# Optimization experiments

Measured on AMD Instinct MI355X. Metric: run time of the kernel, lower is better.

## Reference

```python
import jax, jax.numpy as jnp
import numpy as np

# ---- dims (match init_kwargs) ----
IMG = 128; PATCH = 16; GRID = IMG // PATCH; L = GRID * GRID  # 64 patches
D = 256            # embed_dim
EXP = 2; DIN = D * EXP          # d_inner = 512
DH = 64; H = DIN // DH          # 8 heads
G = 1; N = 64                   # n_groups, d_state
DCONV = 4
DEPTH = 2
NCLS = 1000
BATCH = 16
DINPROJ = 2 * DIN + 2 * G * N + H   # z | xBC | dt
CDIM = DIN + 2 * G * N              # conv channels
EPS = 1e-6

def _snake_indices():
    g = np.arange(L).reshape(GRID, GRID)
    g[1::2] = g[1::2, ::-1]
    return jnp.asarray(g.reshape(-1))

SNAKE = _snake_indices()

def rmsnorm(x, w):
    return x * jax.lax.rsqrt(jnp.mean(x * x, axis=-1, keepdims=True) + EPS) * w

def causal_depthwise_conv(x, w, b):
    # x: (B,L,C), w: (C,K) depthwise causal conv, then SiLU
    xp = jnp.pad(x, ((0, 0), (DCONV - 1, 0), (0, 0)))
    y = sum(xp[:, k:k + x.shape[1], :] * w[:, k] for k in range(DCONV))
    return jax.nn.silu(y + b)

def mamba_block(x, Win, cw, cb, dtb, Alog, Dp, gn, Wout):
    # Mamba-2/3 style selective scan block. x: (B,L,D)
    Bsz, Lx, _ = x.shape
    zxbcdt = x @ Win                                   # (B,L,DINPROJ)
    z   = zxbcdt[..., :DIN]
    xBC = zxbcdt[..., DIN:DIN + CDIM]
    dt  = jax.nn.softplus(zxbcdt[..., DIN + CDIM:] + dtb)   # (B,L,H)
    xBC = causal_depthwise_conv(xBC, cw, cb)
    xs = xBC[..., :DIN].reshape(Bsz, Lx, H, DH)
    Bm = xBC[..., DIN:DIN + G * N].reshape(Bsz, Lx, G, N)
    Cm = xBC[..., DIN + G * N:].reshape(Bsz, Lx, G, N)
    Bh = jnp.repeat(Bm, H // G, axis=2)                # (B,L,H,N)
    Ch = jnp.repeat(Cm, H // G, axis=2)
    decay = jnp.exp(dt * (-jnp.exp(Alog)))             # (B,L,H) in (0,1)
    dBx = jnp.einsum('blh,blhp,blhn->blhpn', dt, xs, Bh)
    def step(h, inp):
        d, u = inp
        h = d[..., None, None] * h + u
        return h, h
    _, hs = jax.lax.scan(step, jnp.zeros((Bsz, H, DH, N), x.dtype),
                         (jnp.moveaxis(decay, 1, 0), jnp.moveaxis(dBx, 1, 0)))
    hs = jnp.moveaxis(hs, 0, 1)                        # (B,L,H,DH,N)
    y = jnp.einsum('blhpn,blhn->blhp', hs, Ch) + Dp[None, None, :, None] * xs
    y = y.reshape(Bsz, Lx, DIN)
    y = rmsnorm(y * jax.nn.silu(z), gn)                # gated RMSNorm
    return y @ Wout                                    # (B,L,D)

def setup_inputs() -> dict:
    key = jax.random.key(0)
    ks = jax.random.split(key, 24)
    s_in = 1.0 / np.sqrt(D); s_out = 1.0 / np.sqrt(DIN)
    def blk(k):
        kk = jax.random.split(k, 8)
        return dict(
            Win=jax.random.normal(kk[0], (DEPTH, D, DINPROJ)) * s_in,
            cw=jax.random.normal(kk[1], (DEPTH, CDIM, DCONV)) * 0.3,
            cb=jnp.zeros((DEPTH, CDIM)),
            dtb=jax.random.normal(kk[2], (DEPTH, H)) * 0.1,
            Alog=jnp.log(jax.random.uniform(kk[3], (DEPTH, H), minval=1.0, maxval=16.0)),
            Dp=jnp.ones((DEPTH, H)),
            gn=jnp.ones((DEPTH, DIN)),
            Wout=jax.random.normal(kk[4], (DEPTH, DIN, D)) * s_out)
    f = blk(ks[0]); b = blk(ks[1])
    inp = {
        'x': jax.random.normal(ks[2], (BATCH, 3, IMG, IMG), dtype=jnp.float32),
        'patch_w': jax.random.normal(ks[3], (D, 3 * PATCH * PATCH)) * (1.0 / np.sqrt(3 * PATCH * PATCH)),
        'patch_b': jnp.zeros((D,)),
        'pos_embed': jax.random.normal(ks[4], (1, L, D)) * 0.02,
        'norms_w': jnp.ones((DEPTH, D)),
        'final_w': jnp.ones((D,)),
        'head_w': jax.random.normal(ks[5], (D, NCLS)) * (1.0 / np.sqrt(D)),
        'head_b': jnp.zeros((NCLS,)),
    }
    for nm, v in f.items():
        inp[nm + '_f'] = v
    for nm, v in b.items():
        inp[nm + '_b'] = v
    return inp

def reference(x, patch_w, patch_b, pos_embed, norms_w, final_w, head_w, head_b,
              Win_f, cw_f, cb_f, dtb_f, Alog_f, Dp_f, gn_f, Wout_f,
              Win_b, cw_b, cb_b, dtb_b, Alog_b, Dp_b, gn_b, Wout_b):
    Bsz = x.shape[0]
    # patch embed == Conv2d(kernel=stride=PATCH)
    p = x.reshape(Bsz, 3, GRID, PATCH, GRID, PATCH).transpose(0, 2, 4, 1, 3, 5)
    p = p.reshape(Bsz, L, 3 * PATCH * PATCH)
    t = p @ patch_w.T + patch_b                        # (B,L,D)
    t = t + pos_embed[0]
    t = t[:, SNAKE, :]                                 # snake scan order
    for i in range(DEPTH):
        nx = rmsnorm(t, norms_w[i])
        of = mamba_block(nx, Win_f[i], cw_f[i], cb_f[i], dtb_f[i], Alog_f[i], Dp_f[i], gn_f[i], Wout_f[i])
        ob = mamba_block(nx[:, ::-1, :], Win_b[i], cw_b[i], cb_b[i], dtb_b[i], Alog_b[i], Dp_b[i], gn_b[i], Wout_b[i])[:, ::-1, :]
        t = t + 0.5 * (of + ob)                        # drop_path_rate=0 -> identity
    t = rmsnorm(t, final_w)
    t = t.mean(axis=1)
    return t @ head_w + head_b
```

## Files before the change

kernel.cpp:

```cpp
#include <hip/hip_runtime.h>
#include <hip/hip_bf16.h>
#include <math.h>

#define IMG 128
#define PATCH 16
#define L 64
#define D 256
#define DIN 512
#define DH 64
#define H 8
#define NSTATE 64
#define DCONV 4
#define DEPTH 2
#define NCLS 1000
#define BATCH 16
#define DINPROJ 1160
#define CDIM 640
#define EPS 1e-6f

typedef __attribute__((ext_vector_type(8))) short short8;
typedef __attribute__((ext_vector_type(4))) float f32x4;
typedef __attribute__((ext_vector_type(4))) unsigned short us4;
typedef unsigned short ushort_t;

__device__ __forceinline__ int snake_tok(int s){
    int r = s >> 3, c = s & 7;
    return (r & 1) ? (r * 8 + (7 - c)) : (r * 8 + c);
}
__device__ __forceinline__ float silu_f(float x){ return x / (1.f + expf(-x)); }
__device__ __forceinline__ float softplus_f(float x){ return x > 20.f ? x : log1pf(expf(x)); }
__device__ __forceinline__ ushort_t f2b(float f){
    __hip_bfloat16 h = __float2bfloat16(f);
    return *(ushort_t*)&h;
}

__device__ __forceinline__ float block_sum256(float v){
    __shared__ float sm[4];
    #pragma unroll
    for (int o = 32; o > 0; o >>= 1) v += __shfl_down(v, o);
    if ((threadIdx.x & 63) == 0) sm[threadIdx.x >> 6] = v;
    __syncthreads();
    return sm[0] + sm[1] + sm[2] + sm[3];
}

__global__ void wconv_k(const float* __restrict__ Win0, const float* __restrict__ Win1,
                        const float* __restrict__ Wout0, const float* __restrict__ Wout1,
                        const float* __restrict__ pw, ushort_t* __restrict__ wbuf){
    int z = blockIdx.z;
    if (z == 8){
        int id = (blockIdx.y * 37 + blockIdx.x) * 256 + threadIdx.x;
        for (; id < 196608; id += 37 * 16 * 256)
            wbuf[id] = f2b(pw[id]);
        return;
    }
    __shared__ float sm[32][33];
    int R, C; const float* src; ushort_t* dst;
    if (z < 4){
        int layer = z >> 1, dir = z & 1;
        src = (dir ? Win1 : Win0) + (size_t)layer * D * DINPROJ;
        dst = wbuf + 196608 + (size_t)z * 296960;
        R = D; C = DINPROJ;
    } else {
        int zz = z - 4, layer = zz >> 1, dir = zz & 1;
        src = (dir ? Wout1 : Wout0) + (size_t)layer * DIN * D;
        dst = wbuf + 1384448 + (size_t)zz * 131072;
        R = DIN; C = D;
    }
    int ctiles = (C + 31) >> 5, rtiles = R >> 5;
    if (blockIdx.x >= ctiles || blockIdx.y >= rtiles) return;
    int c0 = blockIdx.x * 32, r0 = blockIdx.y * 32;
    int tx = threadIdx.x & 31, ty = threadIdx.x >> 5;
    #pragma unroll
    for (int k = 0; k < 4; ++k){
        int r = r0 + ty + 8 * k, c = c0 + tx;
        sm[ty + 8 * k][tx] = (c < C) ? src[(size_t)r * C + c] : 0.f;
    }
    __syncthreads();
    #pragma unroll
    for (int k = 0; k < 4; ++k){
        int dr = c0 + ty + 8 * k, dc = r0 + tx;
        if (dr < C) dst[(size_t)dr * R + dc] = f2b(sm[tx][ty + 8 * k]);
    }
}

__global__ __launch_bounds__(256) void gemm_patch_k(
    const float* __restrict__ x, const ushort_t* __restrict__ Bw,
    float* __restrict__ part)
{
    __shared__ __align__(16) ushort_t As[2][64][40];
    __shared__ __align__(16) ushort_t Bs[2][64][40];
    const int t = threadIdx.x;
    const int n0 = blockIdx.x * 64;
    const int b  = blockIdx.y;
    const int split = blockIdx.z;
    const int kbase = split * 96;
    const int lrow = t >> 2, lc8 = (t & 3) * 8;
    const int tok = snake_tok(lrow), gy = tok >> 3, gx = tok & 7;
    const float* xb = x + (size_t)b * 3 * IMG * IMG;
    const int wave = t >> 6, lane = t & 63;
    const int wm = (wave >> 1) * 32, wn = (wave & 1) * 32;
    const int fro = lane & 15, fk = (lane >> 4) * 8;

    f32x4 acc[2][2];
    #pragma unroll
    for (int i = 0; i < 2; ++i)
        #pragma unroll
        for (int j = 0; j < 2; ++j) acc[i][j] = (f32x4){0.f,0.f,0.f,0.f};

    short8 areg; float4 breg;
    auto gload = [&](int kk){
        int k = kk + lc8;
        int c = k >> 8, rem = k & 255, py = rem >> 4, px = rem & 15;
        const float* src = xb + ((size_t)c * IMG + gy * PATCH + py) * IMG + gx * PATCH + px;
        float4 a0 = *(const float4*)(src);
        float4 a1 = *(const float4*)(src + 4);
        ushort_t tmp[8] = {f2b(a0.x),f2b(a0.y),f2b(a0.z),f2b(a0.w),
                           f2b(a1.x),f2b(a1.y),f2b(a1.z),f2b(a1.w)};
        areg = *(short8*)tmp;
        breg = *(const float4*)(Bw + (size_t)(n0 + lrow) * 768 + kk + lc8);
    };
    auto sstore = [&](int buf){
        *(short8*)&As[buf][lrow][lc8] = areg;
        *(float4*)&Bs[buf][lrow][lc8] = breg;
    };

    const int nk = 3;
    gload(kbase); sstore(0);
    __syncthreads();
    for (int kt = 0; kt < nk; ++kt){
        const int buf = kt & 1;
        if (kt + 1 < nk) gload(kbase + (kt + 1) * 32);
        short8 af[2], bfr[2];
        af[0]  = *(const short8*)&As[buf][wm + fro][fk];
        af[1]  = *(const short8*)&As[buf][wm + 16 + fro][fk];
        bfr[0] = *(const short8*)&Bs[buf][wn + fro][fk];
        bfr[1] = *(const short8*)&Bs[buf][wn + 16 + fro][fk];
        #pragma unroll
        for (int i = 0; i < 2; ++i)
            #pragma unroll
            for (int j = 0; j < 2; ++j)
                acc[i][j] = __builtin_amdgcn_mfma_f32_16x16x32_bf16(af[i], bfr[j], acc[i][j], 0, 0, 0);
        if (kt + 1 < nk) sstore(buf ^ 1);
        __syncthreads();
    }
    float* Cp = part + (size_t)split * (BATCH * L * D);
    #pragma unroll
    for (int i = 0; i < 2; ++i){
        #pragma unroll
        for (int j = 0; j < 2; ++j){
            int col = n0 + wn + j * 16 + (lane & 15);
            #pragma unroll
            for (int r = 0; r < 4; ++r){
                int srow = wm + i * 16 + (lane >> 4) * 4 + r;
                Cp[(size_t)(b * 64 + srow) * D + col] = acc[i][j][r];
            }
        }
    }
}

__global__ void patch_red_k(const float* __restrict__ part, const float* __restrict__ pb,
                            const float* __restrict__ pos, float* __restrict__ t){
    int i = blockIdx.x * 256 + threadIdx.x;
    int d = i & (D - 1), s = (i >> 8) & (L - 1);
    float v = 0.f;
    #pragma unroll
    for (int r = 0; r < 8; ++r) v += part[i + r * (BATCH * L * D)];
    t[i] = v + pb[d] + pos[snake_tok(s) * D + d];
}

__global__ __launch_bounds__(256) void gemm_in_k(
    const float* __restrict__ T, const float* __restrict__ nw,
    const ushort_t* __restrict__ B0, const ushort_t* __restrict__ B1,
    float* __restrict__ C0, float* __restrict__ C1)
{
    __shared__ __align__(16) ushort_t As[64][264];
    __shared__ __align__(16) ushort_t Bs[2][64][40];
    const int dir = blockIdx.z;
    const ushort_t* __restrict__ Bw = dir ? B1 : B0;
    float* __restrict__ C = dir ? C1 : C0;
    const int t = threadIdx.x;
    const int m0 = blockIdx.y * 64, n0 = blockIdx.x * 64;
    const int arow = t >> 2;
    const int wave = t >> 6, lane = t & 63;
    const int wm = (wave >> 1) * 32, wn = (wave & 1) * 32;
    const int fro = lane & 15, fk = (lane >> 4) * 8;

    {
        const float* src = T + (size_t)(m0 + arow) * D;
        float ss = 0.f;
        #pragma unroll
        for (int i = 0; i < 16; ++i){
            int c = (t & 3) * 4 + i * 16;
            float4 v = *(const float4*)(src + c);
            ss += v.x*v.x + v.y*v.y + v.z*v.z + v.w*v.w;
        }
        ss += __shfl_xor(ss, 1);
        ss += __shfl_xor(ss, 2);
        float sc = rsqrtf(ss * (1.f / (float)D) + EPS);
        #pragma unroll
        for (int i = 0; i < 16; ++i){
            int c = (t & 3) * 4 + i * 16;
            float4 v = *(const float4*)(src + c);
            float4 w = *(const float4*)(nw + c);
            us4 o = {f2b(v.x*sc*w.x), f2b(v.y*sc*w.y), f2b(v.z*sc*w.z), f2b(v.w*sc*w.w)};
            *(us4*)&As[arow][c] = o;
        }
    }
    const int lrow = t >> 2, lc8 = (t & 3) * 8;
    float4 breg;
    auto gloadB = [&](int kk){
        int gn = n0 + lrow;
        if (gn < DINPROJ) breg = *(const float4*)(Bw + (size_t)gn * D + kk + lc8);
        else breg = make_float4(0.f,0.f,0.f,0.f);
    };
    auto sstoreB = [&](int buf){ *(float4*)&Bs[buf][lrow][lc8] = breg; };

    f32x4 acc[2][2];
    #pragma unroll
    for (int i = 0; i < 2; ++i)
        #pragma unroll
        for (int j = 0; j < 2; ++j) acc[i][j] = (f32x4){0.f,0.f,0.f,0.f};

    gloadB(0); sstoreB(0);
    __syncthreads();
    const int nk = D / 32;
    for (int kt = 0; kt < nk; ++kt){
        const int buf = kt & 1;
        if (kt + 1 < nk) gloadB((kt + 1) * 32);
        short8 af[2], bfr[2];
        af[0]  = *(const short8*)&As[wm + fro][kt * 32 + fk];
        af[1]  = *(const short8*)&As[wm + 16 + fro][kt * 32 + fk];
        bfr[0] = *(const short8*)&Bs[buf][wn + fro][fk];
        bfr[1] = *(const short8*)&Bs[buf][wn + 16 + fro][fk];
        #pragma unroll
        for (int i = 0; i < 2; ++i)
            #pragma unroll
            for (int j = 0; j < 2; ++j)
                acc[i][j] = __builtin_amdgcn_mfma_f32_16x16x32_bf16(af[i], bfr[j], acc[i][j], 0, 0, 0);
        if (kt + 1 < nk) sstoreB(buf ^ 1);
        __syncthreads();
    }
    #pragma unroll
    for (int i = 0; i < 2; ++i){
        #pragma unroll
        for (int j = 0; j < 2; ++j){
            int col = n0 + wn + j * 16 + (lane & 15);
            if (col >= DINPROJ) continue;
            #pragma unroll
            for (int r = 0; r < 4; ++r){
                int row = m0 + wm + i * 16 + (lane >> 4) * 4 + r;
                C[(size_t)row * DINPROJ + col] = acc[i][j][r];
            }
        }
    }
}

__global__ __launch_bounds__(256) void gemm_out_k(
    const ushort_t* __restrict__ A0, const ushort_t* __restrict__ A1,
    const ushort_t* __restrict__ B0, const ushort_t* __restrict__ B1,
    float* __restrict__ part)
{
    __shared__ __align__(16) ushort_t As[2][64][40];
    __shared__ __align__(16) ushort_t Bs[2][64][40];
    const int t = threadIdx.x;
    const int n0 = blockIdx.x * 64, m0 = blockIdx.y * 64;
    const int z = blockIdx.z;
    const int dir = z >> 2;
    const int kbase = (z & 3) * 128;
    const ushort_t* __restrict__ A = dir ? A1 : A0;
    const ushort_t* __restrict__ B = dir ? B1 : B0;
    const int lrow = t >> 2, lc8 = (t & 3) * 8;
    const int wave = t >> 6, lane = t & 63;
    const int wm = (wave >> 1) * 32, wn = (wave & 1) * 32;
    const int fro = lane & 15, fk = (lane >> 4) * 8;

    float4 areg, breg;
    auto gload = [&](int kk){
        areg = *(const float4*)(A + (size_t)(m0 + lrow) * DIN + kk + lc8);
        breg = *(const float4*)(B + (size_t)(n0 + lrow) * DIN + kk + lc8);
    };
    auto sstore = [&](int buf){
        *(float4*)&As[buf][lrow][lc8] = areg;
        *(float4*)&Bs[buf][lrow][lc8] = breg;
    };

    f32x4 acc[2][2];
    #pragma unroll
    for (int i = 0; i < 2; ++i)
        #pragma unroll
        for (int j = 0; j < 2; ++j) acc[i][j] = (f32x4){0.f,0.f,0.f,0.f};

    const int nk = 4;
    gload(kbase); sstore(0);
    __syncthreads();
    for (int kt = 0; kt < nk; ++kt){
        const int buf = kt & 1;
        if (kt + 1 < nk) gload(kbase + (kt + 1) * 32);
        short8 af[2], bfr[2];
        af[0]  = *(const short8*)&As[buf][wm + fro][fk];
        af[1]  = *(const short8*)&As[buf][wm + 16 + fro][fk];
        bfr[0] = *(const short8*)&Bs[buf][wn + fro][fk];
        bfr[1] = *(const short8*)&Bs[buf][wn + 16 + fro][fk];
        #pragma unroll
        for (int i = 0; i < 2; ++i)
            #pragma unroll
            for (int j = 0; j < 2; ++j)
                acc[i][j] = __builtin_amdgcn_mfma_f32_16x16x32_bf16(af[i], bfr[j], acc[i][j], 0, 0, 0);
        if (kt + 1 < nk) sstore(buf ^ 1);
        __syncthreads();
    }
    float* Cp = part + (size_t)z * (BATCH * L * D);
    #pragma unroll
    for (int i = 0; i < 2; ++i){
        #pragma unroll
        for (int j = 0; j < 2; ++j){
            int col = n0 + wn + j * 16 + (lane & 15);
            #pragma unroll
            for (int r = 0; r < 4; ++r){
                int row = m0 + wm + i * 16 + (lane >> 4) * 4 + r;
                Cp[(size_t)row * D + col] = acc[i][j][r];
            }
        }
    }
}

__global__ void out_red_k(const float* __restrict__ part, float* __restrict__ t){
    int i = blockIdx.x * 256 + threadIdx.x;
    float v = 0.f;
    #pragma unroll
    for (int r = 0; r < 8; ++r) v += part[i + r * (BATCH * L * D)];
    t[i] += 0.5f * v;
}

__global__ void conv_silu_k(const float* __restrict__ zx0, const float* __restrict__ zx1,
                            const float* __restrict__ cw0, const float* __restrict__ cw1,
                            const float* __restrict__ cb0, const float* __restrict__ cb1,
                            float* __restrict__ xy0, float* __restrict__ xy1,
                            float* __restrict__ bc0, float* __restrict__ bc1){
    int dir = blockIdx.z;
    const float* zx = dir ? zx1 : zx0;
    const float* cw = dir ? cw1 : cw0;
    const float* cb = dir ? cb1 : cb0;
    float* xy = dir ? xy1 : xy0;
    float* bc = dir ? bc1 : bc0;
    int s = blockIdx.x, b = blockIdx.y;
    for (int c = threadIdx.x; c < CDIM; c += blockDim.x){
        float acc = cb[c];
        #pragma unroll
        for (int k = 0; k < DCONV; ++k){
            int j = s - (DCONV - 1) + k;
            if (j >= 0){
                int l = dir ? (L - 1 - j) : j;
                acc += cw[c * DCONV + k] * zx[(size_t)(b * L + l) * DINPROJ + DIN + c];
            }
        }
        float v = silu_f(acc);
        if (c < DIN) xy[(size_t)(b * L + s) * DIN + c] = v;
        else         bc[(size_t)(b * L + s) * 128 + (c - DIN)] = v;
    }
}

__global__ __launch_bounds__(512) void yscan2_k(
    const float* __restrict__ zx0, const float* __restrict__ zx1,
    const float* __restrict__ bc0, const float* __restrict__ bc1,
    const float* __restrict__ dtb0, const float* __restrict__ dtb1,
    const float* __restrict__ Al0, const float* __restrict__ Al1,
    const float* __restrict__ Dp0, const float* __restrict__ Dp1,
    float* __restrict__ xy0, float* __restrict__ xy1)
{
    __shared__ float Bc[64][65];
    __shared__ float CX[64][65];
    __shared__ float Am[64][65];
    __shared__ float cumS[64], dtS[64];
    const int h = blockIdx.x, b = blockIdx.y, dir = blockIdx.z;
    const float* zx  = dir ? zx1  : zx0;
    const float* bc  = dir ? bc1  : bc0;
    const float* dtb = dir ? dtb1 : dtb0;
    const float* Al  = dir ? Al1  : Al0;
    const float* Dp  = dir ? Dp1  : Dp0;
    float* xy = dir ? xy1 : xy0;
    const int t = threadIdx.x;

    if (t < 64){
        int s = t, l = dir ? (L - 1 - s) : s;
        float xr = zx[(size_t)(b * L + l) * DINPROJ + DIN + CDIM + h] + dtb[h];
        float dt = softplus_f(xr);
        float val = -expf(Al[h]) * dt;
        #pragma unroll
        for (int o = 1; o < 64; o <<= 1){
            float u = __shfl_up(val, o);
            if (t >= o) val += u;
        }
        cumS[s] = val; dtS[s] = dt;
    }
    for (int i = t; i < 4096; i += 512){
        int s = i >> 6, n = i & 63;
        Bc[s][n] = bc[(size_t)(b * L + s) * 128 + n];
        CX[s][n] = bc[(size_t)(b * L + s) * 128 + 64 + n];
    }
    __syncthreads();
    for (int i = t; i < 4096; i += 512){
        int s = i >> 6, j = i & 63;
        float v = 0.f;
        if (j <= s){
            float acc = 0.f;
            #pragma unroll
            for (int n = 0; n < 64; ++n) acc += CX[s][n] * Bc[j][n];
            v = acc * expf(cumS[s] - cumS[j]) * dtS[j];
        }
        Am[s][j] = v;
    }
    __syncthreads();
    for (int i = t; i < 4096; i += 512){
        int j = i >> 6, p = i & 63;
        CX[j][p] = xy[(size_t)(b * L + j) * DIN + h * DH + p];
    }
    __syncthreads();
    float dp = Dp[h];
    for (int i = t; i < 4096; i += 512){
        int s = i >> 6, p = i & 63;
        float acc = dp * CX[s][p];
        #pragma unroll
        for (int j = 0; j < 64; ++j) acc += Am[s][j] * CX[j][p];
        int l = dir ? (L - 1 - s) : s;
        xy[(size_t)(b * L + l) * DIN + h * DH + p] = acc;
    }
}

__global__ void gate_rmsnorm_k(const float* __restrict__ y0, const float* __restrict__ y1,
                               const float* __restrict__ zx0, const float* __restrict__ zx1,
                               const float* __restrict__ gn0, const float* __restrict__ gn1,
                               ushort_t* __restrict__ ybf0, ushort_t* __restrict__ ybf1){
    int dir = blockIdx.y;
    const float* y = dir ? y1 : y0;
    const float* zx = dir ? zx1 : zx0;
    const float* gn = dir ? gn1 : gn0;
    ushort_t* ybf = dir ? ybf1 : ybf0;
    int row = blockIdx.x;
    float g[2]; float ss = 0.f;
    #pragma unroll
    for (int r = 0; r < 2; ++r){
        int c = threadIdx.x + 256 * r;
        float z = zx[(size_t)row * DINPROJ + c];
        float val = y[(size_t)row * DIN + c] * silu_f(z);
        g[r] = val; ss += val * val;
    }
    float tot = block_sum256(ss);
    float sc = rsqrtf(tot / (float)DIN + EPS);
    #pragma unroll
    for (int r = 0; r < 2; ++r){
        int c = threadIdx.x + 256 * r;
        ybf[(size_t)row * DIN + c] = f2b(g[r] * sc * gn[c]);
    }
}

__global__ __launch_bounds__(1024) void finalmean_k(const float* __restrict__ T,
                                                    const float* __restrict__ fw,
                                                    float* __restrict__ tm){
    __shared__ float part[16][256];
    int b = blockIdx.x;
    int t = threadIdx.x, wave = t >> 6, lane = t & 63;
    float a0 = 0.f, a1 = 0.f, a2 = 0.f, a3 = 0.f;
    for (int s = wave; s < L; s += 16){
        const float* row = T + (size_t)(b * L + s) * D;
        float4 v = *(const float4*)(row + lane * 4);
        float ss = v.x*v.x + v.y*v.y + v.z*v.z + v.w*v.w;
        #pragma unroll
        for (int o = 32; o > 0; o >>= 1) ss += __shfl_xor(ss, o);
        float sc = rsqrtf(ss / (float)D + EPS);
        a0 += v.x * sc; a1 += v.y * sc; a2 += v.z * sc; a3 += v.w * sc;
    }
    *(float4*)&part[wave][lane * 4] = make_float4(a0, a1, a2, a3);
    __syncthreads();
    if (t < 256){
        float v = 0.f;
        #pragma unroll
        for (int w = 0; w < 16; ++w) v += part[w][t];
        tm[b * D + t] = v * (1.f / (float)L) * fw[t];
    }
}

__global__ void head_k(const float* __restrict__ tm, const float* __restrict__ hw,
                       float* __restrict__ hpart){
    int i = blockIdx.x * 256 + threadIdx.x;
    if (i >= BATCH * NCLS) return;
    int z = blockIdx.y;
    int m = i / NCLS, n = i - m * NCLS;
    int k0 = z * 64;
    float a0 = 0.f, a1 = 0.f, a2 = 0.f, a3 = 0.f;
    const float* tr = tm + m * D + k0;
    const float* hc = hw + (size_t)k0 * NCLS + n;
    #pragma unroll 4
    for (int k = 0; k < 64; k += 4){
        a0 = fmaf(tr[k],     hc[(size_t)k * NCLS],       a0);
        a1 = fmaf(tr[k + 1], hc[(size_t)(k + 1) * NCLS], a1);
        a2 = fmaf(tr[k + 2], hc[(size_t)(k + 2) * NCLS], a2);
        a3 = fmaf(tr[k + 3], hc[(size_t)(k + 3) * NCLS], a3);
    }
    hpart[z * (BATCH * NCLS) + i] = (a0 + a1) + (a2 + a3);
}

__global__ void head_red_k(const float* __restrict__ hpart, const float* __restrict__ hb,
                           float* __restrict__ out){
    int i = blockIdx.x * 256 + threadIdx.x;
    if (i >= BATCH * NCLS) return;
    int n = i % NCLS;
    out[i] = hpart[i] + hpart[i + BATCH * NCLS] + hpart[i + 2 * BATCH * NCLS]
           + hpart[i + 3 * BATCH * NCLS] + hb[n];
}

extern "C" void kernel_launch(void* const* d_in, const int* in_sizes, int n_in,
                              void* d_out, int out_size, void* d_ws, size_t ws_size,
                              hipStream_t stream){
    (void)in_sizes; (void)n_in; (void)out_size; (void)ws_size;
    const float* x       = (const float*)d_in[0];
    const float* patch_w = (const float*)d_in[1];
    const float* patch_b = (const float*)d_in[2];
    const float* pos     = (const float*)d_in[3];
    const float* norms_w = (const float*)d_in[4];
    const float* final_w = (const float*)d_in[5];
    const float* head_w  = (const float*)d_in[6];
    const float* head_b  = (const float*)d_in[7];
    const float* Win[2]  = {(const float*)d_in[8],  (const float*)d_in[16]};
    const float* cw[2]   = {(const float*)d_in[9],  (const float*)d_in[17]};
    const float* cb[2]   = {(const float*)d_in[10], (const float*)d_in[18]};
    const float* dtb[2]  = {(const float*)d_in[11], (const float*)d_in[19]};
    const float* Alog[2] = {(const float*)d_in[12], (const float*)d_in[20]};
    const float* Dp[2]   = {(const float*)d_in[13], (const float*)d_in[21]};
    const float* gn[2]   = {(const float*)d_in[14], (const float*)d_in[22]};
    const float* Wout[2] = {(const float*)d_in[15], (const float*)d_in[23]};

    float* ws = (float*)d_ws;
    float* t    = ws;
    float* tm   = t    + 262144;
    float* zx0  = tm   + 4096;
    float* zx1  = zx0  + 1187840;
    float* xy0  = zx1  + 1187840;
    float* xy1  = xy0  + 524288;
    float* bcb0 = xy1  + 524288;
    float* bcb1 = bcb0 + 131072;
    float* f32end = bcb1 + 131072;
    float* part  = zx0;
    float* hpart = xy0;

    ushort_t* ybf0 = (ushort_t*)f32end;
    ushort_t* ybf1 = ybf0 + 524288;
    ushort_t* wbuf = ybf1 + 524288;
    ushort_t* pw_bf   = wbuf;
    ushort_t* win_bf  = wbuf + 196608;
    ushort_t* wout_bf = wbuf + 1384448;

    const int BL = BATCH * L;

    wconv_k<<<dim3(37, 16, 9), 256, 0, stream>>>(
        Win[0], Win[1], Wout[0], Wout[1], patch_w, wbuf);

    gemm_patch_k<<<dim3(4, 16, 8), 256, 0, stream>>>(x, pw_bf, part);
    patch_red_k<<<BL, 256, 0, stream>>>(part, patch_b, pos, t);

    for (int i = 0; i < DEPTH; ++i){
        const float* cw0  = cw[0]   + (size_t)i * CDIM * DCONV;
        const float* cw1  = cw[1]   + (size_t)i * CDIM * DCONV;
        const float* cb0  = cb[0]   + (size_t)i * CDIM;
        const float* cb1  = cb[1]   + (size_t)i * CDIM;
        const float* dtb0 = dtb[0]  + (size_t)i * H;
        const float* dtb1 = dtb[1]  + (size_t)i * H;
        const float* Al0  = Alog[0] + (size_t)i * H;
        const float* Al1  = Alog[1] + (size_t)i * H;
        const float* Dp0  = Dp[0]   + (size_t)i * H;
        const float* Dp1  = Dp[1]   + (size_t)i * H;
        const float* gn0  = gn[0]   + (size_t)i * DIN;
        const float* gn1  = gn[1]   + (size_t)i * DIN;
        const ushort_t* Wi0 = win_bf  + (size_t)(2 * i + 0) * 296960;
        const ushort_t* Wi1 = win_bf  + (size_t)(2 * i + 1) * 296960;
        const ushort_t* Wo0 = wout_bf + (size_t)(2 * i + 0) * 131072;
        const ushort_t* Wo1 = wout_bf + (size_t)(2 * i + 1) * 131072;

        gemm_in_k<<<dim3(19, 16, 2), 256, 0, stream>>>(
            t, norms_w + i * D, Wi0, Wi1, zx0, zx1);
        conv_silu_k<<<dim3(L, BATCH, 2), 256, 0, stream>>>(
            zx0, zx1, cw0, cw1, cb0, cb1, xy0, xy1, bcb0, bcb1);
        yscan2_k<<<dim3(H, BATCH, 2), 512, 0, stream>>>(
            zx0, zx1, bcb0, bcb1, dtb0, dtb1, Al0, Al1, Dp0, Dp1, xy0, xy1);
        gate_rmsnorm_k<<<dim3(BL, 2), 256, 0, stream>>>(
            xy0, xy1, zx0, zx1, gn0, gn1, ybf0, ybf1);
        gemm_out_k<<<dim3(4, 16, 8), 256, 0, stream>>>(ybf0, ybf1, Wo0, Wo1, part);
        out_red_k<<<BL, 256, 0, stream>>>(part, t);
    }

    finalmean_k<<<BATCH, 1024, 0, stream>>>(t, final_w, tm);
    head_k<<<dim3((BATCH * NCLS + 255) / 256, 4), 256, 0, stream>>>(tm, head_w, hpart);
    head_red_k<<<(BATCH * NCLS + 255) / 256, 256, 0, stream>>>(
        hpart, head_b, (float*)d_out);
}
```

Before: 143.8 us.

## Fuse conv into scan, fold final reduction into finalmean, convert patch weights inline

Removes the separate causal conv+SiLU kernel by recomputing the conv for the B/C and x channels inside the scan kernel. The last layer's output-partial reduction is folded into a restructured finalmean kernel, which now produces 8 partial means that head_k sums. Patch weights are converted to bf16 inside the patch GEMM instead of in the weight-conversion kernel. Together these cut launches and intermediate buffers, at the cost of redundant conv recomputation across heads and more global reads in the scan.

```diff
diff --git a/kernel.cpp b/kernel.cpp
--- a/kernel.cpp
+++ b/kernel.cpp
@@ -45,25 +45,19 @@
 
 __global__ void wconv_k(const float* __restrict__ Win0, const float* __restrict__ Win1,
                         const float* __restrict__ Wout0, const float* __restrict__ Wout1,
-                        const float* __restrict__ pw, ushort_t* __restrict__ wbuf){
+                        ushort_t* __restrict__ wbuf){
     int z = blockIdx.z;
-    if (z == 8){
-        int id = (blockIdx.y * 37 + blockIdx.x) * 256 + threadIdx.x;
-        for (; id < 196608; id += 37 * 16 * 256)
-            wbuf[id] = f2b(pw[id]);
-        return;
-    }
     __shared__ float sm[32][33];
     int R, C; const float* src; ushort_t* dst;
     if (z < 4){
         int layer = z >> 1, dir = z & 1;
         src = (dir ? Win1 : Win0) + (size_t)layer * D * DINPROJ;
-        dst = wbuf + 196608 + (size_t)z * 296960;
+        dst = wbuf + (size_t)z * 296960;
         R = D; C = DINPROJ;
     } else {
         int zz = z - 4, layer = zz >> 1, dir = zz & 1;
         src = (dir ? Wout1 : Wout0) + (size_t)layer * DIN * D;
-        dst = wbuf + 1384448 + (size_t)zz * 131072;
+        dst = wbuf + 1187840 + (size_t)zz * 131072;
         R = DIN; C = D;
     }
     int ctiles = (C + 31) >> 5, rtiles = R >> 5;
@@ -84,7 +78,7 @@
 }
 
 __global__ __launch_bounds__(256) void gemm_patch_k(
-    const float* __restrict__ x, const ushort_t* __restrict__ Bw,
+    const float* __restrict__ x, const float* __restrict__ PW,
     float* __restrict__ part)
 {
     __shared__ __align__(16) ushort_t As[2][64][40];
@@ -107,21 +101,26 @@
         #pragma unroll
         for (int j = 0; j < 2; ++j) acc[i][j] = (f32x4){0.f,0.f,0.f,0.f};
 
-    short8 areg; float4 breg;
+    short8 areg, breg;
     auto gload = [&](int kk){
         int k = kk + lc8;
         int c = k >> 8, rem = k & 255, py = rem >> 4, px = rem & 15;
-        const float* src = xb + ((size_t)c * IMG + gy * PATCH + py) * IMG + gx * PATCH + px;
-        float4 a0 = *(const float4*)(src);
-        float4 a1 = *(const float4*)(src + 4);
-        ushort_t tmp[8] = {f2b(a0.x),f2b(a0.y),f2b(a0.z),f2b(a0.w),
-                           f2b(a1.x),f2b(a1.y),f2b(a1.z),f2b(a1.w)};
-        areg = *(short8*)tmp;
-        breg = *(const float4*)(Bw + (size_t)(n0 + lrow) * 768 + kk + lc8);
+        const float* srcA = xb + ((size_t)c * IMG + gy * PATCH + py) * IMG + gx * PATCH + px;
+        float4 a0 = *(const float4*)(srcA);
+        float4 a1 = *(const float4*)(srcA + 4);
+        ushort_t ta[8] = {f2b(a0.x),f2b(a0.y),f2b(a0.z),f2b(a0.w),
+                          f2b(a1.x),f2b(a1.y),f2b(a1.z),f2b(a1.w)};
+        areg = *(short8*)ta;
+        const float* srcB = PW + (size_t)(n0 + lrow) * 768 + kk + lc8;
+        float4 b0 = *(const float4*)(srcB);
+        float4 b1 = *(const float4*)(srcB + 4);
+        ushort_t tb[8] = {f2b(b0.x),f2b(b0.y),f2b(b0.z),f2b(b0.w),
+                          f2b(b1.x),f2b(b1.y),f2b(b1.z),f2b(b1.w)};
+        breg = *(short8*)tb;
     };
     auto sstore = [&](int buf){
         *(short8*)&As[buf][lrow][lc8] = areg;
-        *(float4*)&Bs[buf][lrow][lc8] = breg;
+        *(short8*)&Bs[buf][lrow][lc8] = breg;
     };
 
     const int nk = 3;
@@ -332,37 +331,10 @@
     t[i] += 0.5f * v;
 }
 
-__global__ void conv_silu_k(const float* __restrict__ zx0, const float* __restrict__ zx1,
-                            const float* __restrict__ cw0, const float* __restrict__ cw1,
-                            const float* __restrict__ cb0, const float* __restrict__ cb1,
-                            float* __restrict__ xy0, float* __restrict__ xy1,
-                            float* __restrict__ bc0, float* __restrict__ bc1){
-    int dir = blockIdx.z;
-    const float* zx = dir ? zx1 : zx0;
-    const float* cw = dir ? cw1 : cw0;
-    const float* cb = dir ? cb1 : cb0;
-    float* xy = dir ? xy1 : xy0;
-    float* bc = dir ? bc1 : bc0;
-    int s = blockIdx.x, b = blockIdx.y;
-    for (int c = threadIdx.x; c < CDIM; c += blockDim.x){
-        float acc = cb[c];
-        #pragma unroll
-        for (int k = 0; k < DCONV; ++k){
-            int j = s - (DCONV - 1) + k;
-            if (j >= 0){
-                int l = dir ? (L - 1 - j) : j;
-                acc += cw[c * DCONV + k] * zx[(size_t)(b * L + l) * DINPROJ + DIN + c];
-            }
-        }
-        float v = silu_f(acc);
-        if (c < DIN) xy[(size_t)(b * L + s) * DIN + c] = v;
-        else         bc[(size_t)(b * L + s) * 128 + (c - DIN)] = v;
-    }
-}
-
 __global__ __launch_bounds__(512) void yscan2_k(
     const float* __restrict__ zx0, const float* __restrict__ zx1,
-    const float* __restrict__ bc0, const float* __restrict__ bc1,
+    const float* __restrict__ cw0, const float* __restrict__ cw1,
+    const float* __restrict__ cb0, const float* __restrict__ cb1,
     const float* __restrict__ dtb0, const float* __restrict__ dtb1,
     const float* __restrict__ Al0, const float* __restrict__ Al1,
     const float* __restrict__ Dp0, const float* __restrict__ Dp1,
@@ -374,7 +346,8 @@
     __shared__ float cumS[64], dtS[64];
     const int h = blockIdx.x, b = blockIdx.y, dir = blockIdx.z;
     const float* zx  = dir ? zx1  : zx0;
-    const float* bc  = dir ? bc1  : bc0;
+    const float* cw  = dir ? cw1  : cw0;
+    const float* cb  = dir ? cb1  : cb0;
     const float* dtb = dir ? dtb1 : dtb0;
     const float* Al  = dir ? Al1  : Al0;
     const float* Dp  = dir ? Dp1  : Dp0;
@@ -393,10 +366,21 @@
         }
         cumS[s] = val; dtS[s] = dt;
     }
-    for (int i = t; i < 4096; i += 512){
-        int s = i >> 6, n = i & 63;
-        Bc[s][n] = bc[(size_t)(b * L + s) * 128 + n];
-        CX[s][n] = bc[(size_t)(b * L + s) * 128 + 64 + n];
+    for (int i = t; i < 8192; i += 512){
+        int s = i >> 7, cc = i & 127;
+        int c = DIN + cc;
+        float acc = cb[c];
+        #pragma unroll
+        for (int k = 0; k < DCONV; ++k){
+            int j = s - (DCONV - 1) + k;
+            if (j >= 0){
+                int l = dir ? (L - 1 - j) : j;
+                acc += cw[c * DCONV + k] * zx[(size_t)(b * L + l) * DINPROJ + DIN + c];
+            }
+        }
+        float v = silu_f(acc);
+        if (cc < 64) Bc[s][cc] = v;
+        else         CX[s][cc - 64] = v;
     }
     __syncthreads();
     for (int i = t; i < 4096; i += 512){
@@ -412,8 +396,18 @@
     }
     __syncthreads();
     for (int i = t; i < 4096; i += 512){
-        int j = i >> 6, p = i & 63;
-        CX[j][p] = xy[(size_t)(b * L + j) * DIN + h * DH + p];
+        int s = i >> 6, p = i & 63;
+        int c = h * DH + p;
+        float acc = cb[c];
+        #pragma unroll
+        for (int k = 0; k < DCONV; ++k){
+            int j = s - (DCONV - 1) + k;
+            if (j >= 0){
+                int l = dir ? (L - 1 - j) : j;
+                acc += cw[c * DCONV + k] * zx[(size_t)(b * L + l) * DINPROJ + DIN + c];
+            }
+        }
+        CX[s][p] = silu_f(acc);
     }
     __syncthreads();
     float dp = Dp[h];
@@ -454,42 +448,58 @@
     }
 }
 
-__global__ __launch_bounds__(1024) void finalmean_k(const float* __restrict__ T,
-                                                    const float* __restrict__ fw,
-                                                    float* __restrict__ tm){
-    __shared__ float part[16][256];
-    int b = blockIdx.x;
-    int t = threadIdx.x, wave = t >> 6, lane = t & 63;
+__global__ void finalmean_k(const float* __restrict__ T, const float* __restrict__ part,
+                            const float* __restrict__ fw, float* __restrict__ tm8){
+    __shared__ float sm[4];
+    int b = blockIdx.x, q = blockIdx.y;
+    int d = threadIdx.x;
+    float a = 0.f;
+    for (int r = 0; r < 8; ++r){
+        int row = b * 64 + q * 8 + r;
+        size_t o = (size_t)row * D + d;
+        float pv = 0.f;
+        #pragma unroll
+        for (int u = 0; u < 8; ++u) pv += part[o + (size_t)u * (BATCH * L * D)];
+        float v = T[o] + 0.5f * pv;
+        float ssl = v * v;
+        #pragma unroll
+        for (int off = 32; off > 0; off >>= 1) ssl += __shfl_down(ssl, off);
+        if ((threadIdx.x & 63) == 0) sm[threadIdx.x >> 6] = ssl;
+        __syncthreads();
+        float ss = sm[0] + sm[1] + sm[2] + sm[3];
+        __syncthreads();
+        float sc = rsqrtf(ss / (float)D + EPS);
+        a += v * sc;
+    }
+    tm8[(q * BATCH + b) * D + d] = a * (1.f / (float)L) * fw[d];
+}
+
+__global__ void head_k(const float* __restrict__ tm8, const float* __restrict__ hw,
+                       float* __restrict__ hpart){
+    __shared__ float trs[2][64];
+    int i0 = blockIdx.x * 256;
+    int z = blockIdx.y;
+    int k0 = z * 64;
+    int mmin = i0 / NCLS;
+    int t = threadIdx.x;
+    if (t < 128){
+        int mm = t >> 6, k = t & 63;
+        int m = mmin + mm;
+        float v = 0.f;
+        if (m < BATCH){
+            #pragma unroll
+            for (int q = 0; q < 8; ++q)
+                v += tm8[(q * BATCH + m) * D + k0 + k];
+        }
+        trs[mm][k] = v;
+    }
+    __syncthreads();
+    int i = i0 + t;
+    if (i >= BATCH * NCLS) return;
+    int m = i / NCLS, n = i - m * NCLS;
+    const float* tr = trs[m - mmin];
+    const float* hc = hw + (size_t)k0 * NCLS + n;
     float a0 = 0.f, a1 = 0.f, a2 = 0.f, a3 = 0.f;
-    for (int s = wave; s < L; s += 16){
-        const float* row = T + (size_t)(b * L + s) * D;
-        float4 v = *(const float4*)(row + lane * 4);
-        float ss = v.x*v.x + v.y*v.y + v.z*v.z + v.w*v.w;
-        #pragma unroll
-        for (int o = 32; o > 0; o >>= 1) ss += __shfl_xor(ss, o);
-        float sc = rsqrtf(ss / (float)D + EPS);
-        a0 += v.x * sc; a1 += v.y * sc; a2 += v.z * sc; a3 += v.w * sc;
-    }
-    *(float4*)&part[wave][lane * 4] = make_float4(a0, a1, a2, a3);
-    __syncthreads();
-    if (t < 256){
-        float v = 0.f;
-        #pragma unroll
-        for (int w = 0; w < 16; ++w) v += part[w][t];
-        tm[b * D + t] = v * (1.f / (float)L) * fw[t];
-    }
-}
-
-__global__ void head_k(const float* __restrict__ tm, const float* __restrict__ hw,
-                       float* __restrict__ hpart){
-    int i = blockIdx.x * 256 + threadIdx.x;
-    if (i >= BATCH * NCLS) return;
-    int z = blockIdx.y;
-    int m = i / NCLS, n = i - m * NCLS;
-    int k0 = z * 64;
-    float a0 = 0.f, a1 = 0.f, a2 = 0.f, a3 = 0.f;
-    const float* tr = tm + m * D + k0;
-    const float* hc = hw + (size_t)k0 * NCLS + n;
     #pragma unroll 4
     for (int k = 0; k < 64; k += 4){
         a0 = fmaf(tr[k],     hc[(size_t)k * NCLS],       a0);
@@ -532,30 +542,27 @@
 
     float* ws = (float*)d_ws;
     float* t    = ws;
-    float* tm   = t    + 262144;
-    float* zx0  = tm   + 4096;
+    float* tm8  = t    + 262144;
+    float* zx0  = tm8  + 32768;
     float* zx1  = zx0  + 1187840;
     float* xy0  = zx1  + 1187840;
     float* xy1  = xy0  + 524288;
-    float* bcb0 = xy1  + 524288;
-    float* bcb1 = bcb0 + 131072;
-    float* f32end = bcb1 + 131072;
+    float* f32end = xy1 + 524288;
     float* part  = zx0;
     float* hpart = xy0;
 
     ushort_t* ybf0 = (ushort_t*)f32end;
     ushort_t* ybf1 = ybf0 + 524288;
     ushort_t* wbuf = ybf1 + 524288;
-    ushort_t* pw_bf   = wbuf;
-    ushort_t* win_bf  = wbuf + 196608;
-    ushort_t* wout_bf = wbuf + 1384448;
+    ushort_t* win_bf  = wbuf;
+    ushort_t* wout_bf = wbuf + 1187840;
 
     const int BL = BATCH * L;
 
-    wconv_k<<<dim3(37, 16, 9), 256, 0, stream>>>(
-        Win[0], Win[1], Wout[0], Wout[1], patch_w, wbuf);
-
-    gemm_patch_k<<<dim3(4, 16, 8), 256, 0, stream>>>(x, pw_bf, part);
+    wconv_k<<<dim3(37, 16, 8), 256, 0, stream>>>(
+        Win[0], Win[1], Wout[0], Wout[1], wbuf);
+
+    gemm_patch_k<<<dim3(4, 16, 8), 256, 0, stream>>>(x, patch_w, part);
     patch_red_k<<<BL, 256, 0, stream>>>(part, patch_b, pos, t);
 
     for (int i = 0; i < DEPTH; ++i){
@@ -578,18 +585,17 @@
 
         gemm_in_k<<<dim3(19, 16, 2), 256, 0, stream>>>(
             t, norms_w + i * D, Wi0, Wi1, zx0, zx1);
-        conv_silu_k<<<dim3(L, BATCH, 2), 256, 0, stream>>>(
-            zx0, zx1, cw0, cw1, cb0, cb1, xy0, xy1, bcb0, bcb1);
         yscan2_k<<<dim3(H, BATCH, 2), 512, 0, stream>>>(
-            zx0, zx1, bcb0, bcb1, dtb0, dtb1, Al0, Al1, Dp0, Dp1, xy0, xy1);
+            zx0, zx1, cw0, cw1, cb0, cb1, dtb0, dtb1, Al0, Al1, Dp0, Dp1, xy0, xy1);
         gate_rmsnorm_k<<<dim3(BL, 2), 256, 0, stream>>>(
             xy0, xy1, zx0, zx1, gn0, gn1, ybf0, ybf1);
         gemm_out_k<<<dim3(4, 16, 8), 256, 0, stream>>>(ybf0, ybf1, Wo0, Wo1, part);
-        out_red_k<<<BL, 256, 0, stream>>>(part, t);
-    }
-
-    finalmean_k<<<BATCH, 1024, 0, stream>>>(t, final_w, tm);
-    head_k<<<dim3((BATCH * NCLS + 255) / 256, 4), 256, 0, stream>>>(tm, head_w, hpart);
+        if (i == 0)
+            out_red_k<<<BL, 256, 0, stream>>>(part, t);
+    }
+
+    finalmean_k<<<dim3(BATCH, 8), 256, 0, stream>>>(t, part, final_w, tm8);
+    head_k<<<dim3((BATCH * NCLS + 255) / 256, 4), 256, 0, stream>>>(tm8, head_w, hpart);
     head_red_k<<<(BATCH * NCLS + 255) / 256, 256, 0, stream>>>(
         hpart, head_b, (float*)d_out);
 }
```

Result: slower. 189.6 us (+31.9%).
